# Optimization experiments

Hardware: AMD Instinct MI355X
Metric: run time of the kernel (lower is better)

## Reference

```python
import jax, jax.numpy as jnp
import numpy as np

EPS = 1.1  # GIN epsilon from GINLayer(1.1, dim)
N_GIN = 4

def setup_inputs() -> dict:
    key = jax.random.key(0)
    ks = jax.random.split(key, 24)
    R, F_IN, H1, D = 1048576, 64, 256, 128
    N, E, B, A1, T = 100000, 1600000, 4096, 256, 16
    s = 0.05
    inp = {}
    inp['bulk'] = jax.random.normal(ks[0], (R, F_IN), dtype=jnp.float32)
    inp['seg_ids'] = jnp.sort(jax.random.randint(ks[1], (R,), 0, N))
    inp['edge_src'] = jax.random.randint(ks[2], (E,), 0, N)
    inp['edge_dst'] = jax.random.randint(ks[3], (E,), 0, N)
    inp['root_idx'] = jax.random.randint(ks[4], (B,), 0, N)
    inp['num_nodes'] = N
    # feature extractor: Linear(64,256)+ReLU, Linear(256,128)+ReLU
    inp['W1'] = jax.random.normal(ks[5], (F_IN, H1), dtype=jnp.float32) * s
    inp['b1'] = jnp.zeros((H1,), jnp.float32)
    inp['W2'] = jax.random.normal(ks[6], (H1, D), dtype=jnp.float32) * s
    inp['b2'] = jnp.zeros((D,), jnp.float32)
    # 4 GIN layers, dim D -> D
    inp['gin_W'] = jax.random.normal(ks[7], (N_GIN, D, D), dtype=jnp.float32) * s
    inp['gin_b'] = jnp.zeros((N_GIN, D), jnp.float32)
    # actor: Linear(128,256)+ReLU, Linear(256,16)+ReLU, Softmax
    inp['Wa1'] = jax.random.normal(ks[8], (D, A1), dtype=jnp.float32) * s
    inp['ba1'] = jnp.zeros((A1,), jnp.float32)
    inp['Wa2'] = jax.random.normal(ks[9], (A1, T), dtype=jnp.float32) * s
    inp['ba2'] = jnp.zeros((T,), jnp.float32)
    # critic: Linear(128,256)+ReLU, Linear(256,1)
    inp['Wc1'] = jax.random.normal(ks[10], (D, A1), dtype=jnp.float32) * s
    inp['bc1'] = jnp.zeros((A1,), jnp.float32)
    inp['Wc2'] = jax.random.normal(ks[11], (A1, 1), dtype=jnp.float32) * s
    inp['bc2'] = jnp.zeros((1,), jnp.float32)
    return inp

def reference(bulk, seg_ids, edge_src, edge_dst, root_idx, num_nodes,
              W1, b1, W2, b2, gin_W, gin_b, Wa1, ba1, Wa2, ba2, Wc1, bc1, Wc2, bc2):
    # feature extractor over all rows
    h = jax.nn.relu(bulk @ W1 + b1)
    h = jax.nn.relu(h @ W2 + b2)  # [R, D]
    # per-dataset mean aggregation (self.aggregator over split groups)
    sums = jax.ops.segment_sum(h, seg_ids, num_segments=num_nodes)
    counts = jax.ops.segment_sum(jnp.ones((h.shape[0],), h.dtype), seg_ids, num_segments=num_nodes)
    node_h = sums / jnp.maximum(counts, 1.0)[:, None]  # [N, D]
    # GIN message passing: h_v <- relu(W ((1+eps) h_v + sum_{child u} h_u) + b)
    for i in range(N_GIN):
        agg = jax.ops.segment_sum(node_h[edge_src], edge_dst, num_segments=num_nodes)
        node_h = jax.nn.relu(((1.0 + EPS) * node_h + agg) @ gin_W[i] + gin_b[i])
    X = node_h[root_idx]  # [B, D] current-node representations
    act = jax.nn.softmax(jax.nn.relu(jax.nn.relu(X @ Wa1 + ba1) @ Wa2 + ba2), axis=-1)
    crit = (jax.nn.relu(X @ Wc1 + bc1) @ Wc2 + bc2).squeeze(-1)
    return (act, crit)
```

## Files before the change

### kernel.cpp

```cpp
#include <hip/hip_runtime.h>
#include <math.h>

#define R_ROWS 1048576
#define F_IN   64
#define H1     256
#define D      128
#define NN     100000
#define NE     1600000
#define NB     4096
#define A1     256
#define NTOK   16
#define N_GIN  4
#define FE_ROWS 64

typedef short short8 __attribute__((ext_vector_type(8)));
typedef float f32x4  __attribute__((ext_vector_type(4)));
typedef unsigned int uintx4 __attribute__((ext_vector_type(4)));

__device__ __forceinline__ ushort f2bf(float x) {
    uint u = __builtin_bit_cast(uint, x);
    u += 0x7FFFu + ((u >> 16) & 1u);
    return (ushort)(u >> 16);
}
__device__ __forceinline__ float bf2f(ushort h) {
    uint u = ((uint)h) << 16;
    return __builtin_bit_cast(float, u);
}
__device__ __forceinline__ uint cvtpk(float lo, float hi) {
    uint r;
    asm("v_cvt_pk_bf16_f32 %0, %1, %2" : "=v"(r) : "v"(lo), "v"(hi));
    return r;
}
__device__ __forceinline__ float lo16f(uint p) { return __builtin_bit_cast(float, p << 16); }
__device__ __forceinline__ float hi16f(uint p) { return __builtin_bit_cast(float, p & 0xFFFF0000u); }

__device__ __forceinline__ f32x4 mm(short8 a, short8 b, f32x4 c) {
    return __builtin_amdgcn_mfma_f32_16x16x32_bf16(a, b, c, 0, 0, 0);
}
__device__ __forceinline__ void acc_add(f32x4& L, f32x4& H, const uintx4 p) {
    L[0] += lo16f(p[0]); H[0] += hi16f(p[0]);
    L[1] += lo16f(p[1]); H[1] += hi16f(p[1]);
    L[2] += lo16f(p[2]); H[2] += hi16f(p[2]);
    L[3] += lo16f(p[3]); H[3] += hi16f(p[3]);
}

__device__ __forceinline__ void pack_one(const float* __restrict__ W, int Ndim,
                                         int f, int lane, ushort* __restrict__ out)
{
    const int NTn = Ndim >> 4;
    const int kt = f / NTn, nt = f - kt * NTn;
    const int k0 = kt * 32 + (lane >> 4) * 8;
    const int n = nt * 16 + (lane & 15);
    uintx4 Hv, Lv;
    #pragma unroll
    for (int jj = 0; jj < 4; ++jj) {
        const float x0 = W[(k0 + 2 * jj) * Ndim + n];
        const float x1 = W[(k0 + 2 * jj + 1) * Ndim + n];
        const ushort h0 = f2bf(x0), l0 = f2bf(x0 - bf2f(h0));
        const ushort h1u = f2bf(x1), l1 = f2bf(x1 - bf2f(h1u));
        Hv[jj] = (uint)h0 | ((uint)h1u << 16);
        Lv[jj] = (uint)l0 | ((uint)l1 << 16);
    }
    *reinterpret_cast<uintx4*>(&out[((f * 2 + 0) * 64 + lane) * 8]) = Hv;
    *reinterpret_cast<uintx4*>(&out[((f * 2 + 1) * 64 + lane) * 8]) = Lv;
}

__global__ __launch_bounds__(256) void pack_weights(
    const float* __restrict__ W, int Ndim, int nfrag, ushort* __restrict__ out)
{
    const int id = blockIdx.x * 256 + threadIdx.x;
    const int f = id >> 6, lane = id & 63;
    if (f >= nfrag) return;
    pack_one(W, Ndim, f, lane, out);
}

__global__ __launch_bounds__(256) void pack_gin(
    const float* __restrict__ ginW, ushort* __restrict__ out)
{
    const int l = blockIdx.y;
    const int id = blockIdx.x * 256 + threadIdx.x;
    const int f = id >> 6, lane = id & 63;
    if (f >= 32) return;
    pack_one(ginW + (long)l * D * D, D, f, lane, out + (long)l * 32768);
}

__global__ __launch_bounds__(256, 4) void fe_mfma(
    const float* __restrict__ bulk, const int* __restrict__ seg,
    const ushort* __restrict__ W1p, const float* __restrict__ b1,
    const ushort* __restrict__ W2p, const float* __restrict__ b2,
    float* __restrict__ sums)
{
    __shared__ __align__(16) uint smem_u[10240];
    char* Ab  = (char*)smem_u;
    char* h1b = Ab + 8192;
    float* h2 = (float*)smem_u;

    const int t = threadIdx.x;
    const int lane = t & 63;
    const int w = t >> 6;
    const long r0 = (long)blockIdx.x * FE_ROWS;

    #pragma unroll
    for (int i = 0; i < 4; ++i) {
        const int gid = t + i * 256;
        const int row = gid >> 4;
        const int c4 = (gid & 15) * 4;
        const float4 v = *reinterpret_cast<const float4*>(&bulk[(r0 + row) * F_IN + c4]);
        uint2 pk; pk.x = cvtpk(v.x, v.y); pk.y = cvtpk(v.z, v.w);
        const int byteoff = row * 128 + ((c4 * 2) ^ ((row & 7) << 4));
        *reinterpret_cast<uint2*>(Ab + byteoff) = pk;
    }
    __syncthreads();

    const f32x4 zz = {0.f, 0.f, 0.f, 0.f};
    f32x4 acc1[4][4];
    #pragma unroll
    for (int mtl = 0; mtl < 4; ++mtl)
        #pragma unroll
        for (int ntb = 0; ntb < 4; ++ntb) acc1[mtl][ntb] = zz;

    #pragma unroll
    for (int kt = 0; kt < 2; ++kt) {
        short8 aw[4][2];
        #pragma unroll
        for (int mtl = 0; mtl < 4; ++mtl)
            #pragma unroll
            for (int p = 0; p < 2; ++p) {
                const int f = kt * 16 + (w * 4 + mtl);
                aw[mtl][p] = *reinterpret_cast<const short8*>(&W1p[((f * 2 + p) * 64 + lane) * 8]);
            }
        short8 bh[4];
        #pragma unroll
        for (int ntb = 0; ntb < 4; ++ntb) {
            const int row = ntb * 16 + (lane & 15);
            const int k0 = kt * 32 + (lane >> 4) * 8;
            bh[ntb] = *reinterpret_cast<const short8*>(Ab + (row * 128 + ((k0 * 2) ^ ((row & 7) << 4))));
        }
        #pragma unroll
        for (int mtl = 0; mtl < 4; ++mtl)
            #pragma unroll
            for (int ntb = 0; ntb < 4; ++ntb) {
                acc1[mtl][ntb] = mm(aw[mtl][0], bh[ntb], acc1[mtl][ntb]);
                acc1[mtl][ntb] = mm(aw[mtl][1], bh[ntb], acc1[mtl][ntb]);
            }
    }

    #pragma unroll
    for (int mtl = 0; mtl < 4; ++mtl) {
        const int hcb = w * 64 + mtl * 16 + (lane >> 4) * 4;
        const float4 bv = *reinterpret_cast<const float4*>(&b1[hcb]);
        #pragma unroll
        for (int ntb = 0; ntb < 4; ++ntb) {
            const int hr = (lane & 15) + ntb * 16;
            const float v0 = fmaxf(acc1[mtl][ntb][0] + bv.x, 0.f);
            const float v1 = fmaxf(acc1[mtl][ntb][1] + bv.y, 0.f);
            const float v2 = fmaxf(acc1[mtl][ntb][2] + bv.z, 0.f);
            const float v3 = fmaxf(acc1[mtl][ntb][3] + bv.w, 0.f);
            uint2 pk; pk.x = cvtpk(v0, v1); pk.y = cvtpk(v2, v3);
            const int byteoff = (hr * 512 + hcb * 2) ^ ((hr & 7) << 4);
            *reinterpret_cast<uint2*>(h1b + byteoff) = pk;
        }
    }
    __syncthreads();

    float b2v[2];
    #pragma unroll
    for (int ntl = 0; ntl < 2; ++ntl) b2v[ntl] = b2[w * 32 + ntl * 16 + (lane & 15)];
    f32x4 acc2[4][2];
    #pragma unroll
    for (int mt = 0; mt < 4; ++mt) { acc2[mt][0] = zz; acc2[mt][1] = zz; }

    #pragma unroll
    for (int kt = 0; kt < 8; ++kt) {
        short8 bw2[2][2];
        #pragma unroll
        for (int ntl = 0; ntl < 2; ++ntl)
            #pragma unroll
            for (int p = 0; p < 2; ++p) {
                const int f = kt * 8 + (w * 2 + ntl);
                bw2[ntl][p] = *reinterpret_cast<const short8*>(&W2p[((f * 2 + p) * 64 + lane) * 8]);
            }
        short8 ah[4];
        #pragma unroll
        for (int mt = 0; mt < 4; ++mt) {
            const int row = mt * 16 + (lane & 15);
            const int k0 = kt * 32 + (lane >> 4) * 8;
            ah[mt] = *reinterpret_cast<const short8*>(h1b + ((row * 512 + k0 * 2) ^ ((row & 7) << 4)));
        }
        #pragma unroll
        for (int mt = 0; mt < 4; ++mt)
            #pragma unroll
            for (int ntl = 0; ntl < 2; ++ntl) {
                acc2[mt][ntl] = mm(ah[mt], bw2[ntl][0], acc2[mt][ntl]);
                acc2[mt][ntl] = mm(ah[mt], bw2[ntl][1], acc2[mt][ntl]);
            }
    }
    __syncthreads();

    #pragma unroll
    for (int mt = 0; mt < 4; ++mt)
        #pragma unroll
        for (int ntl = 0; ntl < 2; ++ntl)
            #pragma unroll
            for (int r = 0; r < 4; ++r) {
                const int row = mt * 16 + (lane >> 4) * 4 + r;
                const int col = w * 32 + ntl * 16 + (lane & 15);
                h2[row * 132 + col] = fmaxf(acc2[mt][ntl][r] + b2v[ntl], 0.f);
            }
    __syncthreads();

    {
        const int g = t >> 7;
        const int c = t & 127;
        const int base = g * 32;
        const long rb = r0 + base;
        const int prev = (rb == 0) ? -1 : seg[rb - 1];
        const int nxt = (rb + 32 >= R_ROWS) ? -1 : seg[rb + 32];
        int cur = seg[rb];
        float run = 0.f;
        int runstart = 0;
        #pragma unroll 1
        for (int r = 0; r < 32; ++r) {
            const int s = seg[rb + r];
            if (s != cur) {
                if (runstart != 0 || cur != prev) sums[(long)cur * D + c] = run;
                else atomicAdd(&sums[(long)cur * D + c], run);
                cur = s; run = 0.f; runstart = r;
            }
            run += h2[(base + r) * 132 + c];
        }
        if ((runstart != 0 || cur != prev) && cur != nxt) sums[(long)cur * D + c] = run;
        else atomicAdd(&sums[(long)cur * D + c], run);
    }
}

__global__ __launch_bounds__(256) void start_kernel(const int* __restrict__ seg,
                                                    int* __restrict__ start)
{
    const int n = blockIdx.x * 256 + threadIdx.x;
    if (n > NN) return;
    int lo = 0, hi = R_ROWS;
    #pragma unroll 1
    while (lo < hi) {
        const int mid = (lo + hi) >> 1;
        if (seg[mid] < n) lo = mid + 1; else hi = mid;
    }
    start[n] = lo;
}

__global__ __launch_bounds__(256) void divide_bf(
    const float* __restrict__ sums, const int* __restrict__ start,
    uint* __restrict__ hbf)
{
    const long i = (long)blockIdx.x * 256 + threadIdx.x;
    if (i < (long)NN * 64) {
        const int n = (int)(i >> 6), u = (int)(i & 63);
        const int cA = (u & 15) + (u >> 4) * 32;
        const float inv = 1.f / fmaxf((float)(start[n + 1] - start[n]), 1.f);
        const float vA = sums[(long)n * D + cA] * inv;
        const float vB = sums[(long)n * D + cA + 16] * inv;
        hbf[i] = cvtpk(vA, vB);
    }
}

__global__ __launch_bounds__(256) void hist_kernel(const int* __restrict__ edst,
                                                   int* __restrict__ deg)
{
    const int e = blockIdx.x * 256 + threadIdx.x;
    if (e < NE) atomicAdd(&deg[edst[e]], 1);
}

#define SCHUNK 2048
__global__ __launch_bounds__(256) void scan_reduce(const int* __restrict__ deg,
                                                   int* __restrict__ partials, int n)
{
    __shared__ int sdata[256];
    const int b = blockIdx.x, t = threadIdx.x;
    const int base = b * SCHUNK;
    int sum = 0;
    for (int i = t; i < SCHUNK; i += 256) {
        const int idx = base + i;
        sum += (idx < n) ? deg[idx] : 0;
    }
    sdata[t] = sum; __syncthreads();
    for (int s = 128; s > 0; s >>= 1) {
        if (t < s) sdata[t] += sdata[t + s];
        __syncthreads();
    }
    if (t == 0) partials[b] = sdata[0];
}

__global__ void scan_partials(int* partials, int nb)
{
    if (threadIdx.x == 0) {
        int acc = 0;
        for (int i = 0; i < nb; ++i) { const int v = partials[i]; partials[i] = acc; acc += v; }
    }
}

__global__ __launch_bounds__(256) void scan_write(const int* __restrict__ deg,
                                                  const int* __restrict__ partials,
                                                  int* __restrict__ offsets, int n)
{
    __shared__ int sdata[256];
    const int b = blockIdx.x, t = threadIdx.x;
    const int base = b * SCHUNK;
    int loc[8]; int s = 0;
    #pragma unroll
    for (int j = 0; j < 8; ++j) {
        const int idx = base + t * 8 + j;
        const int v = (idx < n) ? deg[idx] : 0;
        loc[j] = s; s += v;
    }
    sdata[t] = s; __syncthreads();
    for (int d = 1; d < 256; d <<= 1) {
        const int v = (t >= d) ? sdata[t - d] : 0;
        __syncthreads();
        sdata[t] += v;
        __syncthreads();
    }
    const int excl = (t == 0) ? 0 : sdata[t - 1];
    const int tbase = partials[b] + excl;
    #pragma unroll
    for (int j = 0; j < 8; ++j) {
        const int idx = base + t * 8 + j;
        if (idx < n) offsets[idx] = tbase + loc[j];
    }
}

__global__ __launch_bounds__(256) void scatter_edges(const int* __restrict__ esrc,
                                                     const int* __restrict__ edst,
                                                     int* __restrict__ cursor,
                                                     int* __restrict__ csr_src)
{
    const int e = blockIdx.x * 256 + threadIdx.x;
    if (e < NE) {
        const int d = edst[e];
        const int p = atomicAdd(&cursor[d], 1);
        csr_src[p] = esrc[e];
    }
}

__global__ __launch_bounds__(256, 8) void gin_fused(
    const uint* __restrict__ hbf, const int* __restrict__ offsets,
    const int* __restrict__ deg, const int* __restrict__ csr,
    const ushort* __restrict__ Wp, const float* __restrict__ bvec,
    uint* __restrict__ houtbf)
{
    __shared__ __align__(16) char ylds[64 * 256];
    const int t = threadIdx.x, lane = t & 63, w = t >> 6;
    const int q = lane >> 4, m = lane & 15;
    const int r0 = blockIdx.x * 64;

    #pragma unroll 1
    for (int i = 0; i < 16; ++i) {
        const int n = r0 + w * 16 + i;
        const int row = w * 16 + i;
        f32x4 accL = {0.f, 0.f, 0.f, 0.f};
        f32x4 accH = {0.f, 0.f, 0.f, 0.f};
        if (n < NN) {
            const uintx4 sp = *reinterpret_cast<const uintx4*>(&hbf[(long)n * 64 + 4 * m]);
            const float sc = (q == 0) ? 2.1f : 0.f;
            accL[0] = sc * lo16f(sp[0]); accH[0] = sc * hi16f(sp[0]);
            accL[1] = sc * lo16f(sp[1]); accH[1] = sc * hi16f(sp[1]);
            accL[2] = sc * lo16f(sp[2]); accH[2] = sc * hi16f(sp[2]);
            accL[3] = sc * lo16f(sp[3]); accH[3] = sc * hi16f(sp[3]);
            const int off = offsets[n];
            const int dg = deg[n];
            const int dg4 = dg >> 2;
            int jj = 0;
            for (; jj + 4 <= dg4; jj += 4) {
                const int b = off + 4 * jj + q;
                const int s0 = csr[b], s1 = csr[b + 4], s2 = csr[b + 8], s3 = csr[b + 12];
                const uintx4 p0 = *reinterpret_cast<const uintx4*>(&hbf[(long)s0 * 64 + 4 * m]);
                const uintx4 p1 = *reinterpret_cast<const uintx4*>(&hbf[(long)s1 * 64 + 4 * m]);
                const uintx4 p2 = *reinterpret_cast<const uintx4*>(&hbf[(long)s2 * 64 + 4 * m]);
                const uintx4 p3 = *reinterpret_cast<const uintx4*>(&hbf[(long)s3 * 64 + 4 * m]);
                acc_add(accL, accH, p0);
                acc_add(accL, accH, p1);
                acc_add(accL, accH, p2);
                acc_add(accL, accH, p3);
            }
            for (; jj < dg4; ++jj) {
                const int s = csr[off + 4 * jj + q];
                const uintx4 p = *reinterpret_cast<const uintx4*>(&hbf[(long)s * 64 + 4 * m]);
                acc_add(accL, accH, p);
            }
            for (int j = dg4 * 4; j < dg; ++j) {
                if (q == (j & 3)) {
                    const int s = csr[off + j];
                    const uintx4 p = *reinterpret_cast<const uintx4*>(&hbf[(long)s * 64 + 4 * m]);
                    acc_add(accL, accH, p);
                }
            }
        }
        #pragma unroll
        for (int e = 0; e < 4; ++e) {
            accL[e] += __shfl_xor(accL[e], 16);
            accH[e] += __shfl_xor(accH[e], 16);
            accL[e] += __shfl_xor(accL[e], 32);
            accH[e] += __shfl_xor(accH[e], 32);
        }
        const float vA = (q == 0) ? accL[0] : (q == 1) ? accL[1] : (q == 2) ? accL[2] : accL[3];
        const float vB = (q == 0) ? accH[0] : (q == 1) ? accH[1] : (q == 2) ? accH[2] : accH[3];
        const int u = 4 * m + q;
        const int cA = (u & 15) + (u >> 4) * 32;
        const int swz = (row & 7) << 4;
        const uint pk = cvtpk(vA, vB);
        *reinterpret_cast<ushort*>(ylds + ((row * 256 + cA * 2) ^ swz)) = (ushort)pk;
        *reinterpret_cast<ushort*>(ylds + ((row * 256 + (cA + 16) * 2) ^ swz)) = (ushort)(pk >> 16);
    }

    short8 bw0[2][2];
    #pragma unroll
    for (int ntl = 0; ntl < 2; ++ntl)
        #pragma unroll
        for (int p = 0; p < 2; ++p) {
            const int f = w * 2 + ntl;
            bw0[ntl][p] = *reinterpret_cast<const short8*>(&Wp[((f * 2 + p) * 64 + lane) * 8]);
        }
    __syncthreads();

    const f32x4 zz = {0.f, 0.f, 0.f, 0.f};
    f32x4 acc[4][2];
    #pragma unroll
    for (int mt = 0; mt < 4; ++mt) { acc[mt][0] = zz; acc[mt][1] = zz; }

    #pragma unroll
    for (int kt = 0; kt < 4; ++kt) {
        short8 bw[2][2];
        if (kt == 0) {
            #pragma unroll
            for (int ntl = 0; ntl < 2; ++ntl)
                #pragma unroll
                for (int p = 0; p < 2; ++p) bw[ntl][p] = bw0[ntl][p];
        } else {
            #pragma unroll
            for (int ntl = 0; ntl < 2; ++ntl)
                #pragma unroll
                for (int p = 0; p < 2; ++p) {
                    const int f = kt * 8 + (w * 2 + ntl);
                    bw[ntl][p] = *reinterpret_cast<const short8*>(&Wp[((f * 2 + p) * 64 + lane) * 8]);
                }
        }
        #pragma unroll
        for (int mt = 0; mt < 4; ++mt) {
            const int row = mt * 16 + m;
            const int k0 = kt * 32 + q * 8;
            const short8 ah = *reinterpret_cast<const short8*>(
                ylds + ((row * 256 + k0 * 2) ^ ((row & 7) << 4)));
            acc[mt][0] = mm(ah, bw[0][0], acc[mt][0]);
            acc[mt][0] = mm(ah, bw[0][1], acc[mt][0]);
            acc[mt][1] = mm(ah, bw[1][0], acc[mt][1]);
            acc[mt][1] = mm(ah, bw[1][1], acc[mt][1]);
        }
    }

    const float bv0 = bvec[w * 32 + m];
    const float bv1 = bvec[w * 32 + 16 + m];
    #pragma unroll
    for (int mt = 0; mt < 4; ++mt)
        #pragma unroll
        for (int r = 0; r < 4; ++r) {
            const long grow = r0 + mt * 16 + q * 4 + r;
            if (grow < NN) {
                const float v0 = fmaxf(acc[mt][0][r] + bv0, 0.f);
                const float v1 = fmaxf(acc[mt][1][r] + bv1, 0.f);
                houtbf[grow * 64 + w * 16 + m] = cvtpk(v0, v1);
            }
        }
}

__global__ __launch_bounds__(256) void head_kernel(
    const uint* __restrict__ hbf, const int* __restrict__ root,
    const float* __restrict__ Wa1, const float* __restrict__ ba1,
    const float* __restrict__ Wa2, const float* __restrict__ ba2,
    const float* __restrict__ Wc1, const float* __restrict__ bc1,
    const float* __restrict__ Wc2, const float* __restrict__ bc2,
    float* __restrict__ out_act, float* __restrict__ out_crit)
{
    __shared__ float X[D];
    __shared__ float a1[A1];
    __shared__ float red[256];
    __shared__ float logits[NTOK];
    const int t = threadIdx.x;
    const int bi = blockIdx.x;
    const int n = root[bi];
    if (t < 64) {
        const uint p = hbf[(long)n * 64 + t];
        const int cA = (t & 15) + (t >> 4) * 32;
        X[cA] = lo16f(p);
        X[cA + 16] = hi16f(p);
    }
    __syncthreads();

    float acc = ba1[t];
    #pragma unroll
    for (int k = 0; k < D; k += 4) {
        const float4 xv = *reinterpret_cast<const float4*>(&X[k]);
        acc = fmaf(xv.x, Wa1[(k + 0) * A1 + t], acc);
        acc = fmaf(xv.y, Wa1[(k + 1) * A1 + t], acc);
        acc = fmaf(xv.z, Wa1[(k + 2) * A1 + t], acc);
        acc = fmaf(xv.w, Wa1[(k + 3) * A1 + t], acc);
    }
    a1[t] = fmaxf(acc, 0.f);
    __syncthreads();

    const int j = t & 15, p = t >> 4;
    float pa = 0.f;
    #pragma unroll
    for (int k = 0; k < 16; ++k) {
        const int kk = p * 16 + k;
        pa = fmaf(a1[kk], Wa2[kk * NTOK + j], pa);
    }
    red[j * 16 + p] = pa;
    __syncthreads();
    if (t < NTOK) {
        float s = 0.f;
        #pragma unroll
        for (int p2 = 0; p2 < 16; ++p2) s += red[t * 16 + p2];
        logits[t] = fmaxf(s + ba2[t], 0.f);
    }
    __syncthreads();
    if (t < NTOK) {
        float mx = -1e30f;
        #pragma unroll
        for (int i = 0; i < NTOK; ++i) mx = fmaxf(mx, logits[i]);
        red[t] = expf(logits[t] - mx);
    }
    __syncthreads();
    if (t < NTOK) {
        float s = 0.f;
        #pragma unroll
        for (int i = 0; i < NTOK; ++i) s += red[i];
        out_act[(long)bi * NTOK + t] = red[t] / s;
    }
    __syncthreads();

    float accc = bc1[t];
    #pragma unroll
    for (int k = 0; k < D; k += 4) {
        const float4 xv = *reinterpret_cast<const float4*>(&X[k]);
        accc = fmaf(xv.x, Wc1[(k + 0) * A1 + t], accc);
        accc = fmaf(xv.y, Wc1[(k + 1) * A1 + t], accc);
        accc = fmaf(xv.z, Wc1[(k + 2) * A1 + t], accc);
        accc = fmaf(xv.w, Wc1[(k + 3) * A1 + t], accc);
    }
    red[t] = fmaxf(accc, 0.f) * Wc2[t];
    __syncthreads();
    for (int s = 128; s > 0; s >>= 1) {
        if (t < s) red[t] += red[t + s];
        __syncthreads();
    }
    if (t == 0) out_crit[bi] = red[0] + bc2[0];
}

extern "C" void kernel_launch(void* const* d_in, const int* in_sizes, int n_in,
                              void* d_out, int out_size, void* d_ws, size_t ws_size,
                              hipStream_t stream)
{
    const float* bulk = (const float*)d_in[0];
    const int*   seg  = (const int*)d_in[1];
    const int*   esrc = (const int*)d_in[2];
    const int*   edst = (const int*)d_in[3];
    const int*   root = (const int*)d_in[4];
    const float* W1   = (const float*)d_in[6];
    const float* b1   = (const float*)d_in[7];
    const float* W2   = (const float*)d_in[8];
    const float* b2   = (const float*)d_in[9];
    const float* ginW = (const float*)d_in[10];
    const float* ginb = (const float*)d_in[11];
    const float* Wa1  = (const float*)d_in[12];
    const float* ba1  = (const float*)d_in[13];
    const float* Wa2  = (const float*)d_in[14];
    const float* ba2  = (const float*)d_in[15];
    const float* Wc1  = (const float*)d_in[16];
    const float* bc1  = (const float*)d_in[17];
    const float* Wc2  = (const float*)d_in[18];
    const float* bc2  = (const float*)d_in[19];

    char* ws = (char*)d_ws;
    ushort* W1p = (ushort*)ws;
    ushort* W2p = W1p + 32768;
    float* sums    = (float*)(ws + 196608);
    uint*  hbfA    = (uint*)(sums + (long)NN * D);
    uint*  hbfB    = hbfA + (long)NN * 64;
    int*   start   = (int*)(hbfB + (long)NN * 64);
    int*   deg     = start + (NN + 4);
    int*   offsets = deg + NN;
    int*   cursor  = offsets + NN;
    int*   partials= cursor + NN;
    int*   csr     = partials + 256;
    ushort* Gp     = (ushort*)cursor;

    pack_weights<<<8, 256, 0, stream>>>(W1, H1, 32, W1p);
    pack_weights<<<16, 256, 0, stream>>>(W2, D, 64, W2p);

    hipMemsetAsync(sums, 0, (long)NN * D * sizeof(float), stream);
    hipMemsetAsync(deg, 0, NN * sizeof(int), stream);

    fe_mfma<<<R_ROWS / FE_ROWS, 256, 0, stream>>>(bulk, seg, W1p, b1, W2p, b2, sums);
    start_kernel<<<(NN + 256) / 256, 256, 0, stream>>>(seg, start);
    divide_bf<<<((long)NN * 64 + 255) / 256, 256, 0, stream>>>(sums, start, hbfA);

    hist_kernel<<<(NE + 255) / 256, 256, 0, stream>>>(edst, deg);
    const int nchunks = (NN + SCHUNK - 1) / SCHUNK;
    scan_reduce<<<nchunks, 256, 0, stream>>>(deg, partials, NN);
    scan_partials<<<1, 64, 0, stream>>>(partials, nchunks);
    scan_write<<<nchunks, 256, 0, stream>>>(deg, partials, offsets, NN);
    hipMemcpyAsync(cursor, offsets, NN * sizeof(int), hipMemcpyDeviceToDevice, stream);
    scatter_edges<<<(NE + 255) / 256, 256, 0, stream>>>(esrc, edst, cursor, csr);

    pack_gin<<<dim3(8, 4), 256, 0, stream>>>(ginW, Gp);

    uint* hA = hbfA;
    uint* hB = hbfB;
    for (int l = 0; l < N_GIN; ++l) {
        gin_fused<<<(NN + 63) / 64, 256, 0, stream>>>(hA, offsets, deg, csr,
                                                      Gp + (long)l * 32768, ginb + (long)l * D, hB);
        uint* tmp = hA; hA = hB; hB = tmp;
    }

    head_kernel<<<NB, 256, 0, stream>>>(hA, root, Wa1, ba1, Wa2, ba2,
                                        Wc1, bc1, Wc2, bc2,
                                        (float*)d_out, (float*)d_out + (long)NB * NTOK);
}
```

Measured before the change: 848.4 us.

## Compute only root-reachable nodes in final GIN layers

Adds kernels that mark the root nodes and their in-neighbours, then compact them into a list. GIN layer 3 is computed only for those marked nodes, and layer 4 only for the 4096 roots, writing straight into a dense buffer that the head reads. This removes most of the gather and MFMA work in the last two layers. In exchange it adds the mark and compact kernels plus memsets, and layer 3 uses a grid of the full size whose surplus blocks exit early.

```diff
diff --git a/kernel.cpp b/kernel.cpp
--- a/kernel.cpp
+++ b/kernel.cpp
@@ -341,24 +341,64 @@
     }
 }
 
-__global__ __launch_bounds__(256, 8) void gin_fused(
+__global__ __launch_bounds__(256) void mark_kernel(
+    const int* __restrict__ root, const int* __restrict__ offsets,
+    const int* __restrict__ deg, const int* __restrict__ csr,
+    int* __restrict__ mark)
+{
+    const int b = blockIdx.x * 256 + threadIdx.x;
+    if (b < NB) {
+        const int n = root[b];
+        mark[n] = 1;
+        const int off = offsets[n], dg = deg[n];
+        for (int j = 0; j < dg; ++j) mark[csr[off + j]] = 1;
+    }
+}
+
+__global__ __launch_bounds__(256) void compact_kernel(
+    const int* __restrict__ mark, int* __restrict__ list, int* __restrict__ cnt)
+{
+    const int n = blockIdx.x * 256 + threadIdx.x;
+    if (n < NN && mark[n]) {
+        const int p = atomicAdd(cnt, 1);
+        list[p] = n;
+    }
+}
+
+template<int MODE>
+__global__ __launch_bounds__(256, 8) void gin_kernel(
     const uint* __restrict__ hbf, const int* __restrict__ offsets,
     const int* __restrict__ deg, const int* __restrict__ csr,
     const ushort* __restrict__ Wp, const float* __restrict__ bvec,
-    uint* __restrict__ houtbf)
+    uint* __restrict__ outbuf,
+    const int* __restrict__ list, const int* __restrict__ cnt,
+    const int* __restrict__ root)
 {
     __shared__ __align__(16) char ylds[64 * 256];
+    __shared__ int nid[64];
     const int t = threadIdx.x, lane = t & 63, w = t >> 6;
     const int q = lane >> 4, m = lane & 15;
     const int r0 = blockIdx.x * 64;
+    const int CNT = (MODE == 1) ? cnt[0] : 0;
+    if (MODE == 1 && r0 >= CNT) return;
 
     #pragma unroll 1
     for (int i = 0; i < 16; ++i) {
-        const int n = r0 + w * 16 + i;
         const int row = w * 16 + i;
+        int n = -1;
+        if (MODE == 0) {
+            const int nn = r0 + row;
+            if (nn < NN) n = nn;
+        } else if (MODE == 1) {
+            const int idx = r0 + row;
+            if (idx < CNT) n = list[idx];
+        } else {
+            n = root[r0 + row];
+        }
+        if (MODE == 1 && lane == 0) nid[row] = n;
         f32x4 accL = {0.f, 0.f, 0.f, 0.f};
         f32x4 accH = {0.f, 0.f, 0.f, 0.f};
-        if (n < NN) {
+        if (n >= 0) {
             const uintx4 sp = *reinterpret_cast<const uintx4*>(&hbf[(long)n * 64 + 4 * m]);
             const float sc = (q == 0) ? 2.1f : 0.f;
             accL[0] = sc * lo16f(sp[0]); accH[0] = sc * hi16f(sp[0]);
@@ -462,17 +502,26 @@
     for (int mt = 0; mt < 4; ++mt)
         #pragma unroll
         for (int r = 0; r < 4; ++r) {
-            const long grow = r0 + mt * 16 + q * 4 + r;
-            if (grow < NN) {
-                const float v0 = fmaxf(acc[mt][0][r] + bv0, 0.f);
-                const float v1 = fmaxf(acc[mt][1][r] + bv1, 0.f);
-                houtbf[grow * 64 + w * 16 + m] = cvtpk(v0, v1);
+            const int grow_row = mt * 16 + q * 4 + r;
+            const float v0 = fmaxf(acc[mt][0][r] + bv0, 0.f);
+            const float v1 = fmaxf(acc[mt][1][r] + bv1, 0.f);
+            const uint pk = cvtpk(v0, v1);
+            if (MODE == 0) {
+                const long nout = r0 + grow_row;
+                if (nout < NN) outbuf[nout * 64 + w * 16 + m] = pk;
+            } else if (MODE == 1) {
+                if (r0 + grow_row < CNT) {
+                    const long nout = nid[grow_row];
+                    outbuf[nout * 64 + w * 16 + m] = pk;
+                }
+            } else {
+                outbuf[(long)(r0 + grow_row) * 64 + w * 16 + m] = pk;
             }
         }
 }
 
 __global__ __launch_bounds__(256) void head_kernel(
-    const uint* __restrict__ hbf, const int* __restrict__ root,
+    const uint* __restrict__ Xbf, const int* __restrict__ root,
     const float* __restrict__ Wa1, const float* __restrict__ ba1,
     const float* __restrict__ Wa2, const float* __restrict__ ba2,
     const float* __restrict__ Wc1, const float* __restrict__ bc1,
@@ -485,9 +534,8 @@
     __shared__ float logits[NTOK];
     const int t = threadIdx.x;
     const int bi = blockIdx.x;
-    const int n = root[bi];
     if (t < 64) {
-        const uint p = hbf[(long)n * 64 + t];
+        const uint p = Xbf[(long)bi * 64 + t];
         const int cA = (t & 15) + (t >> 4) * 32;
         X[cA] = lo16f(p);
         X[cA + 16] = hi16f(p);
@@ -591,6 +639,10 @@
     int*   cursor  = offsets + NN;
     int*   partials= cursor + NN;
     int*   csr     = partials + 256;
+    int*   mark    = csr + NE;
+    int*   list    = mark + NN;
+    int*   cnt     = list + NN;
+    uint*  Xbf     = (uint*)(cnt + 4);
     ushort* Gp     = (ushort*)cursor;
 
     pack_weights<<<8, 256, 0, stream>>>(W1, H1, 32, W1p);
@@ -598,6 +650,8 @@
 
     hipMemsetAsync(sums, 0, (long)NN * D * sizeof(float), stream);
     hipMemsetAsync(deg, 0, NN * sizeof(int), stream);
+    hipMemsetAsync(mark, 0, NN * sizeof(int), stream);
+    hipMemsetAsync(cnt, 0, sizeof(int), stream);
 
     fe_mfma<<<R_ROWS / FE_ROWS, 256, 0, stream>>>(bulk, seg, W1p, b1, W2p, b2, sums);
     start_kernel<<<(NN + 256) / 256, 256, 0, stream>>>(seg, start);
@@ -611,17 +665,22 @@
     hipMemcpyAsync(cursor, offsets, NN * sizeof(int), hipMemcpyDeviceToDevice, stream);
     scatter_edges<<<(NE + 255) / 256, 256, 0, stream>>>(esrc, edst, cursor, csr);
 
+    mark_kernel<<<(NB + 255) / 256, 256, 0, stream>>>(root, offsets, deg, csr, mark);
+    compact_kernel<<<(NN + 255) / 256, 256, 0, stream>>>(mark, list, cnt);
+
     pack_gin<<<dim3(8, 4), 256, 0, stream>>>(ginW, Gp);
 
-    uint* hA = hbfA;
-    uint* hB = hbfB;
-    for (int l = 0; l < N_GIN; ++l) {
-        gin_fused<<<(NN + 63) / 64, 256, 0, stream>>>(hA, offsets, deg, csr,
-                                                      Gp + (long)l * 32768, ginb + (long)l * D, hB);
-        uint* tmp = hA; hA = hB; hB = tmp;
-    }
-
-    head_kernel<<<NB, 256, 0, stream>>>(hA, root, Wa1, ba1, Wa2, ba2,
+    const int full_grid = (NN + 63) / 64;
+    gin_kernel<0><<<full_grid, 256, 0, stream>>>(hbfA, offsets, deg, csr,
+        Gp + 0L * 32768, ginb + 0L * D, hbfB, list, cnt, root);
+    gin_kernel<0><<<full_grid, 256, 0, stream>>>(hbfB, offsets, deg, csr,
+        Gp + 1L * 32768, ginb + 1L * D, hbfA, list, cnt, root);
+    gin_kernel<1><<<full_grid, 256, 0, stream>>>(hbfA, offsets, deg, csr,
+        Gp + 2L * 32768, ginb + 2L * D, hbfB, list, cnt, root);
+    gin_kernel<2><<<NB / 64, 256, 0, stream>>>(hbfB, offsets, deg, csr,
+        Gp + 3L * 32768, ginb + 3L * D, Xbf, list, cnt, root);
+
+    head_kernel<<<NB, 256, 0, stream>>>(Xbf, root, Wa1, ba1, Wa2, ba2,
                                         Wc1, bc1, Wc2, bc2,
                                         (float*)d_out, (float*)d_out + (long)NB * NTOK);
 }
```

Measured after the change: 845.1 us. About the same (-0.4%).
